# Kernel tuning notes

Measured on AMD Instinct MI355X. Metric: run time of the kernel, lower is better.

## Reference

```python
import jax, jax.numpy as jnp
import numpy as np

N_WORDS = 4096
N_HEADS = 512
EMB = 768          # input_size
HID = 1024         # hidden_size
DIST = 64          # dist_emb_size (forced by Conv1d(64, ...))
SENT_LEN = 64      # fixed sentence length -> static max padded length
PAIR_F = 2 * EMB + DIST  # 1600


def setup_inputs() -> dict:
    key = jax.random.key(0)
    ks = jax.random.split(key, 14)
    words = jax.random.normal(ks[0], (N_WORDS, EMB), dtype=jnp.float32)
    heads_ids = jax.random.randint(ks[1], (N_HEADS,), 0, N_WORDS, dtype=jnp.int64)
    sent_id = (jnp.arange(N_WORDS) // SENT_LEN).astype(jnp.int32)  # sorted, contiguous sentences
    s = 0.02
    return {
        "words": words,
        "heads_ids": heads_ids,
        "sent_id": sent_id,
        "emb_table": jax.random.normal(ks[2], (128, DIST), dtype=jnp.float32) * s,
        "W1": jax.random.normal(ks[3], (PAIR_F, HID), dtype=jnp.float32) * s,
        "b1": jnp.zeros((HID,), jnp.float32),
        "W2": jax.random.normal(ks[4], (HID, 256), dtype=jnp.float32) * s,
        "b2": jnp.zeros((256,), jnp.float32),
        "W3": jax.random.normal(ks[5], (256, DIST), dtype=jnp.float32) * s,
        "b3": jnp.zeros((DIST,), jnp.float32),
        "cw1": jax.random.normal(ks[6], (4, DIST, 3), dtype=jnp.float32) * s,  # Conv1d(64,4,3,1,1)
        "cb1": jnp.zeros((4,), jnp.float32),
        "cw2": jax.random.normal(ks[7], (2, 4, 3), dtype=jnp.float32) * s,    # Conv1d(4,2,3,1,1)
        "cb2": jnp.zeros((2,), jnp.float32),
    }


def _conv1d(x, w, b):
    # x: [N, C_in, L], w: [C_out, C_in, 3], padding=1, stride=1 (torch Conv1d semantics)
    y = jax.lax.conv_general_dilated(x, w, window_strides=(1,), padding=((1, 1),),
                                     dimension_numbers=("NCH", "OIH", "NCH"))
    return y + b[None, :, None]


def reference(words, heads_ids, sent_id, emb_table, W1, b1, W2, b2, W3, b3, cw1, cb1, cw2, cb2):
    n_words = words.shape[0]
    heads = heads_ids.astype(jnp.int32)
    H = heads.shape[0]

    # relative positions & distance-embedding ids, clamped to bucket 127 outside [-63, 63]
    rel = heads[:, None] - jnp.arange(n_words, dtype=jnp.int32)[None, :]      # [H, W]
    eid = rel + 63
    eid = jnp.where((eid < 0) | (eid > 126), 127, eid)

    # per-head sentence span (sent_id is sorted & contiguous)
    sh = sent_id[heads]
    starts = jnp.searchsorted(sent_id, sh, side="left")
    lengths = jnp.searchsorted(sent_id, sh, side="right") - starts            # [H]

    # padded ragged layout: row i holds words of head i's sentence, left-packed
    j = jnp.arange(SENT_LEN, dtype=jnp.int32)
    cols = starts[:, None] + j[None, :]                                       # [H, L]
    mask = j[None, :] < lengths[:, None]                                      # [H, L]
    cols_c = jnp.clip(cols, 0, n_words - 1)

    head_w = words[heads]                                                     # [H, E]
    col_w = words[cols_c]                                                     # [H, L, E]
    dist = emb_table[jnp.take_along_axis(eid, cols_c, axis=1)]                # [H, L, DIST]
    feat = jnp.concatenate(
        [jnp.broadcast_to(head_w[:, None, :], col_w.shape), col_w, dist], axis=-1)
    feat = jnp.where(mask[..., None], feat, jnp.zeros((), feat.dtype))        # zero padding rows (as torch)

    # FFNN (dropout is identity in eval mode)
    x = jax.nn.relu(feat @ W1 + b1)
    x = jax.nn.relu(x @ W2 + b2)
    x = x @ W3 + b3                                                           # [H, L, 64]

    # conv stack over the padded ragged axis
    x = _conv1d(x.transpose(0, 2, 1), cw1, cb1)
    x = _conv1d(x, cw2, cb2)
    res = x.transpose(0, 2, 1)                                                # [H, L, 2]

    # scatter back into [H, n_words, 2]; masked slots get out-of-range col -> dropped
    rows = jnp.broadcast_to(jnp.arange(H, dtype=jnp.int32)[:, None], mask.shape)
    cols_sc = jnp.where(mask, cols, n_words)
    scores = jnp.full((H, n_words, 2), -jnp.inf, dtype=words.dtype)
    scores = scores.at[rows, cols_sc].set(res, mode="drop")

    # eval-mode validity log-mask
    valid_starts = jnp.log((rel >= 0).astype(words.dtype))
    valid_ends = jnp.log((rel <= 0).astype(words.dtype))
    valid = jnp.stack([valid_starts, valid_ends], axis=2)
    return scores + valid
```

## Files before the change

kernel.cpp:

```cpp
#include <hip/hip_runtime.h>
#include <math.h>

#define NW   4096
#define NH   512
#define EMBD 768
#define HIDD 1024
#define DISTD 64
#define SLEN 64

#define NEG_BIG (-1.0e30f)

typedef __attribute__((ext_vector_type(8))) short short8;
typedef __attribute__((ext_vector_type(16))) float f32x16;
typedef __attribute__((ext_vector_type(4))) float f32x4;

#define MFMA32(a, b, c) __builtin_amdgcn_mfma_f32_32x32x16_bf16((a), (b), (c), 0, 0, 0)
#define MFMA16(a, b, c) __builtin_amdgcn_mfma_f32_16x16x32_bf16((a), (b), (c), 0, 0, 0)

__device__ __forceinline__ unsigned short f2bf(float f) {
    unsigned u = __float_as_uint(f);
    u += 0x7FFFu + ((u >> 16) & 1u);
    return (unsigned short)(u >> 16);
}
__device__ __forceinline__ float bf2f(unsigned short s) {
    return __uint_as_float(((unsigned)s) << 16);
}
__device__ __forceinline__ unsigned cvtpk(float lo, float hi) {
    unsigned r;
    asm("v_cvt_pk_bf16_f32 %0, %1, %2" : "=v"(r) : "v"(lo), "v"(hi));
    return r;
}
__device__ __forceinline__ short8 pack8(float f0, float f1, float f2, float f3,
                                        float f4, float f5, float f6, float f7) {
    union { unsigned u[4]; short8 s; } r;
    r.u[0] = cvtpk(f0, f1); r.u[1] = cvtpk(f2, f3);
    r.u[2] = cvtpk(f4, f5); r.u[3] = cvtpk(f6, f7);
    return r.s;
}

#define BARL()                                                   \
    do {                                                         \
        asm volatile("s_waitcnt lgkmcnt(0)" ::: "memory");       \
        __builtin_amdgcn_s_barrier();                            \
    } while (0)

__device__ __forceinline__ void pack_b32_dev(long t, const float* __restrict__ src,
                                             int ld, int nb32, int KB,
                                             unsigned short* __restrict__ dst)
{
    int l = (int)(t & 63); long u = t >> 6;
    int nb = (int)(u % nb32); int kb = (int)(u / nb32);
    int row0 = kb * 16 + ((l >> 5) << 3);
    int col  = (nb << 5) + (l & 31);
    const float* s = src + (size_t)row0 * ld + col;
    short8 v;
#pragma unroll
    for (int j = 0; j < 8; ++j) v[j] = (short)f2bf(s[(size_t)j * ld]);
    *(short8*)(dst + (((size_t)nb * KB + kb) << 9) + l * 8) = v;
}

__device__ __forceinline__ void pack_b16_dev(long t, const float* __restrict__ src,
                                             int ld, int nb16, int KB,
                                             unsigned short* __restrict__ dst)
{
    int l = (int)(t & 63); long u = t >> 6;
    int nb = (int)(u % nb16); int kb = (int)(u / nb16);
    int row0 = kb * 32 + ((l >> 4) << 3);
    int col  = (nb << 4) + (l & 15);
    const float* s = src + (size_t)row0 * ld + col;
    short8 v;
#pragma unroll
    for (int j = 0; j < 8; ++j) v[j] = (short)f2bf(s[(size_t)j * ld]);
    *(short8*)(dst + (((size_t)nb * KB + kb) << 9) + l * 8) = v;
}

__device__ __forceinline__ void cvt8_dev(long i, const float* __restrict__ src,
                                         unsigned short* __restrict__ dst)
{
    const float* s = src + i * 8;
    short8 v;
#pragma unroll
    for (int j = 0; j < 8; ++j) v[j] = (short)f2bf(s[j]);
    *(short8*)(dst + i * 8) = v;
}

#define WPS 776
__global__ __launch_bounds__(256)
void prep_kernel(const float* __restrict__ words, const float* __restrict__ emb,
                 const float* __restrict__ W1, const float* __restrict__ W2,
                 const float* __restrict__ W3,
                 const int* __restrict__ heads, const int* __restrict__ sent_id,
                 unsigned short* __restrict__ wpack, unsigned short* __restrict__ embb,
                 unsigned short* __restrict__ W1pa, unsigned short* __restrict__ W1px,
                 unsigned short* __restrict__ W1pd,
                 unsigned short* __restrict__ W2p, unsigned short* __restrict__ W3p,
                 int* __restrict__ starts, int* __restrict__ lens)
{
    __shared__ unsigned short tls[32 * WPS];

    const int b = blockIdx.x, tid = threadIdx.x;
    if (b < 128) {
        const int m = b;
#pragma unroll
        for (int i = 0; i < 24; ++i) {
            const int idx = tid + i * 256;
            const int r = idx / 192, c4 = (idx % 192) * 4;
            float4 v = *(const float4*)(words + ((size_t)(m * 32 + r)) * EMBD + c4);
            tls[r * WPS + c4 + 0] = f2bf(v.x);
            tls[r * WPS + c4 + 1] = f2bf(v.y);
            tls[r * WPS + c4 + 2] = f2bf(v.z);
            tls[r * WPS + c4 + 3] = f2bf(v.w);
        }
        __syncthreads();
        const int l = tid & 63, w = tid >> 6;
        for (int kb = w; kb < 48; kb += 4) {
            short8 v = *(const short8*)&tls[(l & 31) * WPS + kb * 16 + ((l >> 5) << 3)];
            *(short8*)(wpack + (((size_t)m * 48 + kb) << 9) + l * 8) = v;
        }
    } else if (b < 132) {
        cvt8_dev((long)(b - 128) * 256 + tid, emb, embb);
    } else if (b < 516) {
        pack_b32_dev((long)(b - 132) * 256 + tid, W1, HIDD, 32, 48, W1pa);
    } else if (b < 900) {
        pack_b32_dev((long)(b - 516) * 256 + tid, W1 + (size_t)768 * HIDD, HIDD, 32, 48, W1px);
    } else if (b < 932) {
        pack_b32_dev((long)(b - 900) * 256 + tid, W1 + (size_t)1536 * HIDD, HIDD, 32, 4, W1pd);
    } else if (b < 1060) {
        pack_b32_dev((long)(b - 932) * 256 + tid, W2, 256, 8, 64, W2p);
    } else if (b < 1068) {
        pack_b16_dev((long)(b - 1060) * 256 + tid, W3, 64, 4, 8, W3p);
    } else {
        int h = (b - 1068) * 256 + tid;
        if (h < NH) {
            int head = heads[h];
            int s = sent_id[head];
            int lo = 0, hi = NW;
            while (lo < hi) { int mid = (lo + hi) >> 1; if (sent_id[mid] < s) lo = mid + 1; else hi = mid; }
            int start = lo;
            lo = 0; hi = NW;
            while (lo < hi) { int mid = (lo + hi) >> 1; if (sent_id[mid] <= s) lo = mid + 1; else hi = mid; }
            int len = lo - start;
            if (len > SLEN) len = SLEN;
            starts[h] = start;
            lens[h] = len;
        }
    }
}

__global__ __launch_bounds__(256, 4)
void gemms_kernel(const unsigned short* __restrict__ wpack,
                  const unsigned short* __restrict__ embb,
                  const unsigned short* __restrict__ W1pa,
                  const unsigned short* __restrict__ W1px,
                  const unsigned short* __restrict__ W1pd,
                  const float* __restrict__ b1, const int* __restrict__ heads,
                  unsigned short* __restrict__ XwP, unsigned short* __restrict__ Hcb,
                  unsigned short* __restrict__ Dtb)
{
    __shared__ unsigned short tls[4][32 * 40];

    const int b = blockIdx.x, tid = threadIdx.x;
    const int l = tid & 63, w = tid >> 6;

    if (b < 1024) {
        const int mB = b >> 3, nB = b & 7;
        const int cbg = nB * 4 + w;
        const unsigned short* ap = wpack + (((size_t)mB * 48) << 9) + l * 8;
        const unsigned short* bp = W1px + (((size_t)cbg * 48) << 9) + l * 8;
        f32x16 acc = {};
#pragma unroll
        for (int kk = 0; kk < 48; ++kk) {
            short8 a = *(const short8*)(ap + ((size_t)kk << 9));
            short8 bb = *(const short8*)(bp + ((size_t)kk << 9));
            acc = MFMA32(a, bb, acc);
        }
        const int col = cbg * 32 + (l & 31);
        const float bv = b1[col];
        unsigned short* tw = tls[w];
#pragma unroll
        for (int r = 0; r < 16; ++r) {
            int rowl = (r & 3) + 8 * (r >> 2) + 4 * (l >> 5);
            tw[rowl * 40 + (l & 31)] = f2bf(acc[r] + bv);
        }
        short8 v0 = *(const short8*)&tw[(l & 31) * 40 + ((l >> 5) << 3)];
        short8 v1 = *(const short8*)&tw[(l & 31) * 40 + 16 + ((l >> 5) << 3)];
        *(short8*)(XwP + (((size_t)(mB * 64 + cbg * 2)) << 9) + l * 8) = v0;
        *(short8*)(XwP + (((size_t)(mB * 64 + cbg * 2 + 1)) << 9) + l * 8) = v1;
    } else if (b < 1152) {
        const int q = b - 1024;
        const int mB = q >> 3, nB = q & 7;
        const int cbg = nB * 4 + w;
        int row = heads[mB * 32 + (l & 31)];
        const unsigned short* ap = wpack + (((size_t)(row >> 5) * 48) << 9)
                                 + ((row & 31) + 32 * (l >> 5)) * 8;
        const unsigned short* bp = W1pa + (((size_t)cbg * 48) << 9) + l * 8;
        f32x16 acc = {};
#pragma unroll
        for (int kk = 0; kk < 48; ++kk) {
            short8 a = *(const short8*)(ap + ((size_t)kk << 9));
            short8 bb = *(const short8*)(bp + ((size_t)kk << 9));
            acc = MFMA32(a, bb, acc);
        }
        const int col = cbg * 32 + (l & 31);
#pragma unroll
        for (int r = 0; r < 16; ++r) {
            int rr = mB * 32 + (r & 3) + 8 * (r >> 2) + 4 * (l >> 5);
            Hcb[(size_t)rr * HIDD + col] = f2bf(acc[r]);
        }
    } else {
        const int q = b - 1152;
        const int mB = q >> 3, nB = q & 7;
        const int cbg = nB * 4 + w;
        const unsigned short* ap = embb + (size_t)(mB * 32 + (l & 31)) * DISTD + ((l >> 5) << 3);
        const unsigned short* bp = W1pd + (((size_t)cbg * 4) << 9) + l * 8;
        f32x16 acc = {};
#pragma unroll
        for (int kk = 0; kk < 4; ++kk) {
            short8 a = *(const short8*)(ap + kk * 16);
            short8 bb = *(const short8*)(bp + ((size_t)kk << 9));
            acc = MFMA32(a, bb, acc);
        }
        const int col = cbg * 32 + (l & 31);
#pragma unroll
        for (int r = 0; r < 16; ++r) {
            int rr = mB * 32 + (r & 3) + 8 * (r >> 2) + 4 * (l >> 5);
            Dtb[(size_t)rr * HIDD + col] = f2bf(acc[r]);
        }
    }
}

__global__ __launch_bounds__(256)
void packd_kernel(const unsigned short* __restrict__ Dtb,
                  unsigned short* __restrict__ PDr)
{
    const int tid = threadIdx.x, l = tid & 63;
    const int c = blockIdx.x * 4 + (tid >> 6);
    const int s = c / 192, rem = c % 192;
    const int m = rem >> 6, kb = rem & 63;
    const int row = 126 - (s + 32 * m + (l & 31));
    const int koff = kb * 16 + ((l >> 5) << 3);
    short8 v = *(const short8*)(Dtb + (size_t)row * HIDD + koff);
    *(short8*)(PDr + ((size_t)c << 9) + l * 8) = v;
}

#define NT 32
__global__ __launch_bounds__(512)
void head_kernel(const unsigned short* __restrict__ XwP,
                 const unsigned short* __restrict__ Hcb,
                 const unsigned short* __restrict__ PDr,
                 const unsigned short* __restrict__ W2p,
                 const float* __restrict__ b2,
                 const unsigned short* __restrict__ W3p,
                 const float* __restrict__ b3,
                 const float* __restrict__ cw1, const float* __restrict__ cb1,
                 const float* __restrict__ cw2, const float* __restrict__ cb2,
                 const int* __restrict__ heads, const int* __restrict__ starts,
                 const int* __restrict__ lens,
                 float* __restrict__ out)
{
    __shared__ char smem[67584];
    unsigned short* Ast = (unsigned short*)smem;
    unsigned short* Bst = (unsigned short*)(smem + 16384);
    unsigned short* x2s = (unsigned short*)smem;
    float* x3s = (float*)smem;
    float* y1s = (float*)(smem + 35328);
    float* y2s = (float*)(smem + 37376);

    const int tid = threadIdx.x;
    const int l = tid & 63, w = tid >> 6;
    const int h0 = blockIdx.x * 2;

    const int head0 = heads[h0],  head1 = heads[h0 + 1];
    const int strt0 = starts[h0], strt1 = starts[h0 + 1];
    const int len0  = lens[h0],   len1  = lens[h0 + 1];

    const int kkA = w >> 2, rb = w & 3;
    const int hbA = rb >> 1;
    const int headA = hbA ? head1 : head0;
    const int strtA = hbA ? strt1 : strt0;
    const int q0A = 63 - (headA - strtA);
    const unsigned short* xwPp =
        XwP + (((size_t)((strtA >> 5) + (rb & 1)) * 64) << 9) + l * 8;
    const unsigned short* ddPp =
        PDr + (((size_t)((q0A & 31) * 3 + (q0A >> 5) + (rb & 1)) * 64) << 9) + l * 8;
    const unsigned short* hcp = Hcb + (size_t)(h0 + hbA) * HIDD + ((l >> 5) << 3);
    const int kkB = w >> 2, nbB0 = (w & 3) * 2;
    const int mb = w & 1, nq = w >> 1;

    f32x16 acc[2][2] = {};

    short8 rxw, rhc, rdd, rb0, rb1;

#define LOADT(t)                                                              \
    {                                                                         \
        const int kb_ = (t) * 2 + kkA;                                        \
        rxw = *(const short8*)(xwPp + ((size_t)kb_ << 9));                    \
        rdd = *(const short8*)(ddPp + ((size_t)kb_ << 9));                    \
        rhc = *(const short8*)(hcp + kb_ * 16);                               \
        const size_t c0_ = ((size_t)(nbB0 * 64 + (t) * 2 + kkB)) << 9;        \
        rb0 = *(const short8*)(W2p + c0_ + l * 8);                            \
        rb1 = *(const short8*)(W2p + c0_ + 32768 + l * 8);                    \
    }

#define WRITET(t)                                                             \
    {                                                                         \
        const int buf_ = (t) & 1;                                             \
        float f_[8];                                                          \
        _Pragma("unroll")                                                     \
        for (int j = 0; j < 8; ++j)                                           \
            f_[j] = fmaxf(bf2f((unsigned short)rxw[j])                        \
                        + bf2f((unsigned short)rhc[j])                        \
                        + bf2f((unsigned short)rdd[j]), 0.f);                 \
        short8 v_ = pack8(f_[0], f_[1], f_[2], f_[3], f_[4], f_[5], f_[6], f_[7]); \
        *(short8*)&Ast[buf_ * 4096 + (kkA * 4 + rb) * 512 + l * 8] = v_;      \
        *(short8*)&Bst[buf_ * 8192 + (kkB * 8 + nbB0) * 512 + l * 8] = rb0;   \
        *(short8*)&Bst[buf_ * 8192 + (kkB * 8 + nbB0 + 1) * 512 + l * 8] = rb1; \
    }

    LOADT(0);
    WRITET(0);
    LOADT(1);
    BARL();

#pragma unroll 2
    for (int t = 0; t < NT; ++t) {
        const int buf = t & 1;
        short8 af0[2], af1[2], bf0[2], bf1[2];
#pragma unroll
        for (int k2 = 0; k2 < 2; ++k2) {
            af0[k2] = *(const short8*)&Ast[buf * 4096 + (k2 * 4 + mb * 2 + 0) * 512 + l * 8];
            af1[k2] = *(const short8*)&Ast[buf * 4096 + (k2 * 4 + mb * 2 + 1) * 512 + l * 8];
            bf0[k2] = *(const short8*)&Bst[buf * 8192 + (k2 * 8 + nq * 2 + 0) * 512 + l * 8];
            bf1[k2] = *(const short8*)&Bst[buf * 8192 + (k2 * 8 + nq * 2 + 1) * 512 + l * 8];
        }
        if (t + 1 < NT) WRITET(t + 1);
        if (t + 2 < NT) LOADT(t + 2);
        __builtin_amdgcn_s_setprio(1);
#pragma unroll
        for (int k2 = 0; k2 < 2; ++k2) {
            acc[0][0] = MFMA32(af0[k2], bf0[k2], acc[0][0]);
            acc[0][1] = MFMA32(af0[k2], bf1[k2], acc[0][1]);
            acc[1][0] = MFMA32(af1[k2], bf0[k2], acc[1][0]);
            acc[1][1] = MFMA32(af1[k2], bf1[k2], acc[1][1]);
        }
        __builtin_amdgcn_s_setprio(0);
        BARL();
    }

#pragma unroll
    for (int i = 0; i < 2; ++i) {
#pragma unroll
        for (int n = 0; n < 2; ++n) {
            const int ct = nq * 64 + n * 32 + (l & 31);
            const float bv = b2[ct];
#pragma unroll
            for (int r = 0; r < 16; ++r) {
                const int rt = mb * 64 + i * 32 + (r & 3) + 8 * (r >> 2) + 4 * (l >> 5);
                const int hb = rt >> 6, rl = rt & 63;
                x2s[hb * 16896 + rl * 264 + ct] = f2bf(fmaxf(acc[i][n][r] + bv, 0.f));
            }
        }
    }
    __syncthreads();

    {
        const int hb = w >> 2, q = w & 3;
        const unsigned short* x2h = x2s + hb * 16896;
        f32x4 acc2[4] = {};
#pragma unroll
        for (int kk = 0; kk < 8; ++kk) {
            short8 bf = *(const short8*)(W3p + ((q * 8 + kk) << 9) + l * 8);
#pragma unroll
            for (int mi = 0; mi < 4; ++mi) {
                short8 af = *(const short8*)&x2h[(mi * 16 + (l & 15)) * 264 + kk * 32 + ((l >> 4) << 3)];
                acc2[mi] = MFMA16(af, bf, acc2[mi]);
            }
        }
        __syncthreads();
        float* x3h = x3s + hb * 4416;
        const int col = q * 16 + (l & 15);
        const float b3v = b3[col];
#pragma unroll
        for (int mi = 0; mi < 4; ++mi) {
#pragma unroll
            for (int r = 0; r < 4; ++r) {
                const int rowv = mi * 16 + (l >> 4) * 4 + r;
                x3h[rowv * 69 + col] = acc2[mi][r] + b3v;
            }
        }
    }
    __syncthreads();

    {
        const int hb3 = tid >> 8;
        const int co = (tid >> 6) & 3;
        const int ll = tid & 63;
        const float* x3h = x3s + hb3 * 4416;
        float s = cb1[co];
        const float* wb = cw1 + co * DISTD * 3;
        for (int ci = 0; ci < DISTD; ++ci) {
            float w0 = wb[ci * 3 + 0], w1 = wb[ci * 3 + 1], w2v = wb[ci * 3 + 2];
            float xm = (ll > 0) ? x3h[(ll - 1) * 69 + ci] : 0.f;
            float xc = x3h[ll * 69 + ci];
            float xp = (ll < 63) ? x3h[(ll + 1) * 69 + ci] : 0.f;
            s = fmaf(xm, w0, s);
            s = fmaf(xc, w1, s);
            s = fmaf(xp, w2v, s);
        }
        y1s[hb3 * 256 + co * 64 + ll] = s;
    }
    __syncthreads();

    if (tid < 256) {
        const int hb4 = tid >> 7;
        const int co = (tid >> 6) & 1;
        const int ll = tid & 63;
        const float* yh = y1s + hb4 * 256;
        const int head = hb4 ? head1 : head0;
        const int strt = hb4 ? strt1 : strt0;
        float s = cb2[co];
#pragma unroll
        for (int ci = 0; ci < 4; ++ci) {
            const float* wb = cw2 + (co * 4 + ci) * 3;
            const float* yr = yh + ci * 64;
            float xm = (ll > 0) ? yr[ll - 1] : 0.f;
            float xc = yr[ll];
            float xp = (ll < 63) ? yr[ll + 1] : 0.f;
            s = fmaf(xm, wb[0], s);
            s = fmaf(xc, wb[1], s);
            s = fmaf(xp, wb[2], s);
        }
        const int col = strt + ll;
        const int rel = head - col;
        const bool valid = (co == 0) ? (rel >= 0) : (rel <= 0);
        y2s[hb4 * 128 + ll * 2 + co] = valid ? s : NEG_BIG;
    }
    __syncthreads();

    {
        const int hb = tid >> 8;
        const int c8 = tid & 255;
        const int strt = hb ? strt1 : strt0;
        const int len  = hb ? len1  : len0;
        float* orow = out + ((size_t)(h0 + hb) * NW) * 2;
        const float* yh = y2s + hb * 128;
#pragma unroll
        for (int i = 0; i < 16; ++i) {
            const int col = i * 256 + c8;
            float2 v;
            if (col >= strt && col < strt + len) {
                v = *(const float2*)&yh[(col - strt) * 2];
            } else {
                v.x = NEG_BIG; v.y = NEG_BIG;
            }
            *(float2*)&orow[(size_t)col * 2] = v;
        }
    }
}

extern "C" void kernel_launch(void* const* d_in, const int* in_sizes, int n_in,
                              void* d_out, int out_size, void* d_ws, size_t ws_size,
                              hipStream_t stream)
{
    const float* words = (const float*)d_in[0];
    const int* heads   = (const int*)d_in[1];
    const int* sent_id = (const int*)d_in[2];
    const float* emb   = (const float*)d_in[3];
    const float* W1    = (const float*)d_in[4];
    const float* b1    = (const float*)d_in[5];
    const float* W2    = (const float*)d_in[6];
    const float* b2    = (const float*)d_in[7];
    const float* W3    = (const float*)d_in[8];
    const float* b3    = (const float*)d_in[9];
    const float* cw1   = (const float*)d_in[10];
    const float* cb1   = (const float*)d_in[11];
    const float* cw2   = (const float*)d_in[12];
    const float* cb2   = (const float*)d_in[13];
    float* out = (float*)d_out;

    char* wsb = (char*)d_ws;
    unsigned short* XwP  = (unsigned short*)(wsb + 0);
    unsigned short* Hcb  = (unsigned short*)(wsb + 8388608);
    unsigned short* Dtb  = (unsigned short*)(wsb + 9437184);
    unsigned short* W2p  = (unsigned short*)(wsb + 9699328);
    unsigned short* W3p  = (unsigned short*)(wsb + 10223616);
    unsigned short* PDr  = (unsigned short*)(wsb + 10256384);
    unsigned short* embb = (unsigned short*)(wsb + 16547840);
    int* starts          = (int*)(wsb + 16564224);
    int* lens            = (int*)(wsb + 16566272);
    char* ob = (char*)d_out;
    unsigned short* wpack  = (unsigned short*)(ob + 0);
    unsigned short* W1pa   = (unsigned short*)(ob + 6291456);
    unsigned short* W1px   = (unsigned short*)(ob + 7864320);
    unsigned short* W1pd   = (unsigned short*)(ob + 9437184);
    (void)ws_size; (void)in_sizes; (void)n_in; (void)out_size;

    prep_kernel<<<dim3(1070), dim3(256), 0, stream>>>(
        words, emb, W1, W2, W3, heads, sent_id,
        wpack, embb, W1pa, W1px, W1pd, W2p, W3p, starts, lens);

    gemms_kernel<<<dim3(1184), dim3(256), 0, stream>>>(
        wpack, embb, W1pa, W1px, W1pd, b1, heads, XwP, Hcb, Dtb);

    packd_kernel<<<dim3(1536), dim3(256), 0, stream>>>(Dtb, PDr);

    head_kernel<<<dim3(NH / 2), dim3(512), 0, stream>>>(
        XwP, Hcb, PDr, W2p, b2, W3p, b3, cw1, cb1, cw2, cb2,
        heads, starts, lens, out);
}
```

Baseline: 77.68 us.

## Process one head per block instead of two in head_kernel

The head kernel now assigns one head per 512-thread block and launches 512 blocks instead of 256. Shared memory is cut to about 40KB and launch bounds request 4 blocks per CU, so more of the GPU's CUs are filled and occupancy rises. In exchange, each block streams the full W2 tile for only 64 rows, which doubles W2 traffic and halves MFMA work per B load. Half the waves also sit idle during A-tile prep and the W3 stage.

```diff
diff --git a/kernel.cpp b/kernel.cpp
--- a/kernel.cpp
+++ b/kernel.cpp
@@ -244,7 +244,7 @@
 }
 
 #define NT 32
-__global__ __launch_bounds__(512)
+__global__ __launch_bounds__(512, 4)
 void head_kernel(const unsigned short* __restrict__ XwP,
                  const unsigned short* __restrict__ Hcb,
                  const unsigned short* __restrict__ PDr,
@@ -258,61 +258,61 @@
                  const int* __restrict__ lens,
                  float* __restrict__ out)
 {
-    __shared__ char smem[67584];
+    __shared__ char smem[40960];
     unsigned short* Ast = (unsigned short*)smem;
-    unsigned short* Bst = (unsigned short*)(smem + 16384);
+    unsigned short* Bst = (unsigned short*)(smem + 8192);
     unsigned short* x2s = (unsigned short*)smem;
     float* x3s = (float*)smem;
-    float* y1s = (float*)(smem + 35328);
-    float* y2s = (float*)(smem + 37376);
+    float* y1s = (float*)(smem + 17664);
+    float* y2s = (float*)(smem + 18688);
 
     const int tid = threadIdx.x;
     const int l = tid & 63, w = tid >> 6;
-    const int h0 = blockIdx.x * 2;
-
-    const int head0 = heads[h0],  head1 = heads[h0 + 1];
-    const int strt0 = starts[h0], strt1 = starts[h0 + 1];
-    const int len0  = lens[h0],   len1  = lens[h0 + 1];
-
-    const int kkA = w >> 2, rb = w & 3;
-    const int hbA = rb >> 1;
-    const int headA = hbA ? head1 : head0;
-    const int strtA = hbA ? strt1 : strt0;
-    const int q0A = 63 - (headA - strtA);
+    const int h = blockIdx.x;
+
+    const int head = heads[h];
+    const int strt = starts[h];
+    const int len  = lens[h];
+
+    const int kkA = (w >> 1) & 1, rbA = w & 1;
+    const int q0 = 63 - (head - strt);
     const unsigned short* xwPp =
-        XwP + (((size_t)((strtA >> 5) + (rb & 1)) * 64) << 9) + l * 8;
+        XwP + (((size_t)((strt >> 5) + rbA) * 64) << 9) + l * 8;
     const unsigned short* ddPp =
-        PDr + (((size_t)((q0A & 31) * 3 + (q0A >> 5) + (rb & 1)) * 64) << 9) + l * 8;
-    const unsigned short* hcp = Hcb + (size_t)(h0 + hbA) * HIDD + ((l >> 5) << 3);
+        PDr + (((size_t)((q0 & 31) * 3 + (q0 >> 5) + rbA) * 64) << 9) + l * 8;
+    const unsigned short* hcp = Hcb + (size_t)h * HIDD + ((l >> 5) << 3);
     const int kkB = w >> 2, nbB0 = (w & 3) * 2;
-    const int mb = w & 1, nq = w >> 1;
-
-    f32x16 acc[2][2] = {};
-
+    const int rbC = w & 1, ncC = w >> 1;
+
+    f32x16 acc[2] = {};
     short8 rxw, rhc, rdd, rb0, rb1;
 
 #define LOADT(t)                                                              \
     {                                                                         \
-        const int kb_ = (t) * 2 + kkA;                                        \
-        rxw = *(const short8*)(xwPp + ((size_t)kb_ << 9));                    \
-        rdd = *(const short8*)(ddPp + ((size_t)kb_ << 9));                    \
-        rhc = *(const short8*)(hcp + kb_ * 16);                               \
-        const size_t c0_ = ((size_t)(nbB0 * 64 + (t) * 2 + kkB)) << 9;        \
-        rb0 = *(const short8*)(W2p + c0_ + l * 8);                            \
-        rb1 = *(const short8*)(W2p + c0_ + 32768 + l * 8);                    \
+        if (w < 4) {                                                          \
+            const int kbA_ = (t) * 2 + kkA;                                   \
+            rxw = *(const short8*)(xwPp + ((size_t)kbA_ << 9));               \
+            rdd = *(const short8*)(ddPp + ((size_t)kbA_ << 9));               \
+            rhc = *(const short8*)(hcp + kbA_ * 16);                          \
+        }                                                                     \
+        const int kbB_ = (t) * 2 + kkB;                                       \
+        rb0 = *(const short8*)(W2p + (((size_t)(nbB0 * 64 + kbB_)) << 9) + l * 8); \
+        rb1 = *(const short8*)(W2p + (((size_t)((nbB0 + 1) * 64 + kbB_)) << 9) + l * 8); \
     }
 
 #define WRITET(t)                                                             \
     {                                                                         \
         const int buf_ = (t) & 1;                                             \
-        float f_[8];                                                          \
-        _Pragma("unroll")                                                     \
-        for (int j = 0; j < 8; ++j)                                           \
-            f_[j] = fmaxf(bf2f((unsigned short)rxw[j])                        \
-                        + bf2f((unsigned short)rhc[j])                        \
-                        + bf2f((unsigned short)rdd[j]), 0.f);                 \
-        short8 v_ = pack8(f_[0], f_[1], f_[2], f_[3], f_[4], f_[5], f_[6], f_[7]); \
-        *(short8*)&Ast[buf_ * 4096 + (kkA * 4 + rb) * 512 + l * 8] = v_;      \
+        if (w < 4) {                                                          \
+            float f_[8];                                                      \
+            _Pragma("unroll")                                                 \
+            for (int j = 0; j < 8; ++j)                                       \
+                f_[j] = fmaxf(bf2f((unsigned short)rxw[j])                    \
+                            + bf2f((unsigned short)rhc[j])                    \
+                            + bf2f((unsigned short)rdd[j]), 0.f);             \
+            short8 v_ = pack8(f_[0], f_[1], f_[2], f_[3], f_[4], f_[5], f_[6], f_[7]); \
+            *(short8*)&Ast[buf_ * 2048 + (kkA * 2 + rbA) * 512 + l * 8] = v_; \
+        }                                                                     \
         *(short8*)&Bst[buf_ * 8192 + (kkB * 8 + nbB0) * 512 + l * 8] = rb0;   \
         *(short8*)&Bst[buf_ * 8192 + (kkB * 8 + nbB0 + 1) * 512 + l * 8] = rb1; \
     }
@@ -325,104 +325,92 @@
 #pragma unroll 2
     for (int t = 0; t < NT; ++t) {
         const int buf = t & 1;
-        short8 af0[2], af1[2], bf0[2], bf1[2];
+        short8 af[2], bf0[2], bf1[2];
 #pragma unroll
         for (int k2 = 0; k2 < 2; ++k2) {
-            af0[k2] = *(const short8*)&Ast[buf * 4096 + (k2 * 4 + mb * 2 + 0) * 512 + l * 8];
-            af1[k2] = *(const short8*)&Ast[buf * 4096 + (k2 * 4 + mb * 2 + 1) * 512 + l * 8];
-            bf0[k2] = *(const short8*)&Bst[buf * 8192 + (k2 * 8 + nq * 2 + 0) * 512 + l * 8];
-            bf1[k2] = *(const short8*)&Bst[buf * 8192 + (k2 * 8 + nq * 2 + 1) * 512 + l * 8];
+            af[k2]  = *(const short8*)&Ast[buf * 2048 + (k2 * 2 + rbC) * 512 + l * 8];
+            bf0[k2] = *(const short8*)&Bst[buf * 8192 + (k2 * 8 + ncC * 2 + 0) * 512 + l * 8];
+            bf1[k2] = *(const short8*)&Bst[buf * 8192 + (k2 * 8 + ncC * 2 + 1) * 512 + l * 8];
         }
         if (t + 1 < NT) WRITET(t + 1);
         if (t + 2 < NT) LOADT(t + 2);
         __builtin_amdgcn_s_setprio(1);
 #pragma unroll
         for (int k2 = 0; k2 < 2; ++k2) {
-            acc[0][0] = MFMA32(af0[k2], bf0[k2], acc[0][0]);
-            acc[0][1] = MFMA32(af0[k2], bf1[k2], acc[0][1]);
-            acc[1][0] = MFMA32(af1[k2], bf0[k2], acc[1][0]);
-            acc[1][1] = MFMA32(af1[k2], bf1[k2], acc[1][1]);
+            acc[0] = MFMA32(af[k2], bf0[k2], acc[0]);
+            acc[1] = MFMA32(af[k2], bf1[k2], acc[1]);
         }
         __builtin_amdgcn_s_setprio(0);
         BARL();
     }
 
 #pragma unroll
-    for (int i = 0; i < 2; ++i) {
-#pragma unroll
-        for (int n = 0; n < 2; ++n) {
-            const int ct = nq * 64 + n * 32 + (l & 31);
-            const float bv = b2[ct];
-#pragma unroll
-            for (int r = 0; r < 16; ++r) {
-                const int rt = mb * 64 + i * 32 + (r & 3) + 8 * (r >> 2) + 4 * (l >> 5);
-                const int hb = rt >> 6, rl = rt & 63;
-                x2s[hb * 16896 + rl * 264 + ct] = f2bf(fmaxf(acc[i][n][r] + bv, 0.f));
+    for (int n = 0; n < 2; ++n) {
+        const int ct = ncC * 64 + n * 32 + (l & 31);
+        const float bv = b2[ct];
+#pragma unroll
+        for (int r = 0; r < 16; ++r) {
+            const int rt = rbC * 32 + (r & 3) + 8 * (r >> 2) + 4 * (l >> 5);
+            x2s[rt * 264 + ct] = f2bf(fmaxf(acc[n][r] + bv, 0.f));
+        }
+    }
+    __syncthreads();
+
+    {
+        f32x4 acc2[4] = {};
+        if (w < 4) {
+#pragma unroll
+            for (int kk = 0; kk < 8; ++kk) {
+                short8 bfr = *(const short8*)(W3p + ((w * 8 + kk) << 9) + l * 8);
+#pragma unroll
+                for (int mi = 0; mi < 4; ++mi) {
+                    short8 afr = *(const short8*)&x2s[(mi * 16 + (l & 15)) * 264 + kk * 32 + ((l >> 4) << 3)];
+                    acc2[mi] = MFMA16(afr, bfr, acc2[mi]);
+                }
             }
         }
+        __syncthreads();
+        if (w < 4) {
+            const int col = w * 16 + (l & 15);
+            const float b3v = b3[col];
+#pragma unroll
+            for (int mi = 0; mi < 4; ++mi) {
+#pragma unroll
+                for (int r = 0; r < 4; ++r) {
+                    const int rowv = mi * 16 + (l >> 4) * 4 + r;
+                    x3s[rowv * 69 + col] = acc2[mi][r] + b3v;
+                }
+            }
+        }
     }
     __syncthreads();
 
-    {
-        const int hb = w >> 2, q = w & 3;
-        const unsigned short* x2h = x2s + hb * 16896;
-        f32x4 acc2[4] = {};
-#pragma unroll
-        for (int kk = 0; kk < 8; ++kk) {
-            short8 bf = *(const short8*)(W3p + ((q * 8 + kk) << 9) + l * 8);
-#pragma unroll
-            for (int mi = 0; mi < 4; ++mi) {
-                short8 af = *(const short8*)&x2h[(mi * 16 + (l & 15)) * 264 + kk * 32 + ((l >> 4) << 3)];
-                acc2[mi] = MFMA16(af, bf, acc2[mi]);
-            }
-        }
-        __syncthreads();
-        float* x3h = x3s + hb * 4416;
-        const int col = q * 16 + (l & 15);
-        const float b3v = b3[col];
-#pragma unroll
-        for (int mi = 0; mi < 4; ++mi) {
-#pragma unroll
-            for (int r = 0; r < 4; ++r) {
-                const int rowv = mi * 16 + (l >> 4) * 4 + r;
-                x3h[rowv * 69 + col] = acc2[mi][r] + b3v;
-            }
-        }
-    }
-    __syncthreads();
-
-    {
-        const int hb3 = tid >> 8;
-        const int co = (tid >> 6) & 3;
+    if (tid < 256) {
+        const int co = tid >> 6;
         const int ll = tid & 63;
-        const float* x3h = x3s + hb3 * 4416;
         float s = cb1[co];
         const float* wb = cw1 + co * DISTD * 3;
         for (int ci = 0; ci < DISTD; ++ci) {
             float w0 = wb[ci * 3 + 0], w1 = wb[ci * 3 + 1], w2v = wb[ci * 3 + 2];
-            float xm = (ll > 0) ? x3h[(ll - 1) * 69 + ci] : 0.f;
-            float xc = x3h[ll * 69 + ci];
-            float xp = (ll < 63) ? x3h[(ll + 1) * 69 + ci] : 0.f;
+            float xm = (ll > 0) ? x3s[(ll - 1) * 69 + ci] : 0.f;
+            float xc = x3s[ll * 69 + ci];
+            float xp = (ll < 63) ? x3s[(ll + 1) * 69 + ci] : 0.f;
             s = fmaf(xm, w0, s);
             s = fmaf(xc, w1, s);
             s = fmaf(xp, w2v, s);
         }
-        y1s[hb3 * 256 + co * 64 + ll] = s;
+        y1s[co * 64 + ll] = s;
     }
     __syncthreads();
 
-    if (tid < 256) {
-        const int hb4 = tid >> 7;
-        const int co = (tid >> 6) & 1;
+    if (tid < 128) {
+        const int co = tid >> 6;
         const int ll = tid & 63;
-        const float* yh = y1s + hb4 * 256;
-        const int head = hb4 ? head1 : head0;
-        const int strt = hb4 ? strt1 : strt0;
         float s = cb2[co];
 #pragma unroll
         for (int ci = 0; ci < 4; ++ci) {
             const float* wb = cw2 + (co * 4 + ci) * 3;
-            const float* yr = yh + ci * 64;
+            const float* yr = y1s + ci * 64;
             float xm = (ll > 0) ? yr[ll - 1] : 0.f;
             float xc = yr[ll];
             float xp = (ll < 63) ? yr[ll + 1] : 0.f;
@@ -433,23 +421,18 @@
         const int col = strt + ll;
         const int rel = head - col;
         const bool valid = (co == 0) ? (rel >= 0) : (rel <= 0);
-        y2s[hb4 * 128 + ll * 2 + co] = valid ? s : NEG_BIG;
+        y2s[ll * 2 + co] = valid ? s : NEG_BIG;
     }
     __syncthreads();
 
     {
-        const int hb = tid >> 8;
-        const int c8 = tid & 255;
-        const int strt = hb ? strt1 : strt0;
-        const int len  = hb ? len1  : len0;
-        float* orow = out + ((size_t)(h0 + hb) * NW) * 2;
-        const float* yh = y2s + hb * 128;
-#pragma unroll
-        for (int i = 0; i < 16; ++i) {
-            const int col = i * 256 + c8;
+        float* orow = out + ((size_t)h * NW) * 2;
+#pragma unroll
+        for (int i = 0; i < 8; ++i) {
+            const int col = i * 512 + tid;
             float2 v;
             if (col >= strt && col < strt + len) {
-                v = *(const float2*)&yh[(col - strt) * 2];
+                v = *(const float2*)&y2s[(col - strt) * 2];
             } else {
                 v.x = NEG_BIG; v.y = NEG_BIG;
             }
@@ -504,7 +487,7 @@
 
     packd_kernel<<<dim3(1536), dim3(256), 0, stream>>>(Dtb, PDr);
 
-    head_kernel<<<dim3(NH / 2), dim3(512), 0, stream>>>(
+    head_kernel<<<dim3(NH), dim3(512), 0, stream>>>(
         XwP, Hcb, PDr, W2p, b2, W3p, b3, cw1, cb1, cw2, cb2,
         heads, starts, lens, out);
 }
```

Result: slower. 80.43 us (+3.5%).

## Drop packd kernel, read distance rows directly, move W2/W3 packing into gemms

Applied to the files above, without the earlier changes.

Removes the packd_kernel launch that repacked the distance-projection table into MFMA fragment layout. The head kernel now loads distance fragments straight from the row-major Dtb, using a reversed row index and a 16-element k stride. The W2/W3 packing and the sentence-span search move from prep_kernel into extra blocks of gemms_kernel, and the s_setprio hints around the MFMA loop are removed. This saves one launch and a 6MB intermediate, at the cost of less-coalesced strided global loads in the head kernel's inner loop.

```diff
diff --git a/kernel.cpp b/kernel.cpp
--- a/kernel.cpp
+++ b/kernel.cpp
@@ -87,14 +87,10 @@
 #define WPS 776
 __global__ __launch_bounds__(256)
 void prep_kernel(const float* __restrict__ words, const float* __restrict__ emb,
-                 const float* __restrict__ W1, const float* __restrict__ W2,
-                 const float* __restrict__ W3,
-                 const int* __restrict__ heads, const int* __restrict__ sent_id,
+                 const float* __restrict__ W1,
                  unsigned short* __restrict__ wpack, unsigned short* __restrict__ embb,
                  unsigned short* __restrict__ W1pa, unsigned short* __restrict__ W1px,
-                 unsigned short* __restrict__ W1pd,
-                 unsigned short* __restrict__ W2p, unsigned short* __restrict__ W3p,
-                 int* __restrict__ starts, int* __restrict__ lens)
+                 unsigned short* __restrict__ W1pd)
 {
     __shared__ unsigned short tls[32 * WPS];
 
@@ -123,27 +119,8 @@
         pack_b32_dev((long)(b - 132) * 256 + tid, W1, HIDD, 32, 48, W1pa);
     } else if (b < 900) {
         pack_b32_dev((long)(b - 516) * 256 + tid, W1 + (size_t)768 * HIDD, HIDD, 32, 48, W1px);
-    } else if (b < 932) {
+    } else {
         pack_b32_dev((long)(b - 900) * 256 + tid, W1 + (size_t)1536 * HIDD, HIDD, 32, 4, W1pd);
-    } else if (b < 1060) {
-        pack_b32_dev((long)(b - 932) * 256 + tid, W2, 256, 8, 64, W2p);
-    } else if (b < 1068) {
-        pack_b16_dev((long)(b - 1060) * 256 + tid, W3, 64, 4, 8, W3p);
-    } else {
-        int h = (b - 1068) * 256 + tid;
-        if (h < NH) {
-            int head = heads[h];
-            int s = sent_id[head];
-            int lo = 0, hi = NW;
-            while (lo < hi) { int mid = (lo + hi) >> 1; if (sent_id[mid] < s) lo = mid + 1; else hi = mid; }
-            int start = lo;
-            lo = 0; hi = NW;
-            while (lo < hi) { int mid = (lo + hi) >> 1; if (sent_id[mid] <= s) lo = mid + 1; else hi = mid; }
-            int len = lo - start;
-            if (len > SLEN) len = SLEN;
-            starts[h] = start;
-            lens[h] = len;
-        }
     }
 }
 
@@ -153,9 +130,13 @@
                   const unsigned short* __restrict__ W1pa,
                   const unsigned short* __restrict__ W1px,
                   const unsigned short* __restrict__ W1pd,
+                  const float* __restrict__ W2, const float* __restrict__ W3,
                   const float* __restrict__ b1, const int* __restrict__ heads,
+                  const int* __restrict__ sent_id,
                   unsigned short* __restrict__ XwP, unsigned short* __restrict__ Hcb,
-                  unsigned short* __restrict__ Dtb)
+                  unsigned short* __restrict__ Dtb,
+                  unsigned short* __restrict__ W2p, unsigned short* __restrict__ W3p,
+                  int* __restrict__ starts, int* __restrict__ lens)
 {
     __shared__ unsigned short tls[4][32 * 40];
 
@@ -207,7 +188,7 @@
             int rr = mB * 32 + (r & 3) + 8 * (r >> 2) + 4 * (l >> 5);
             Hcb[(size_t)rr * HIDD + col] = f2bf(acc[r]);
         }
-    } else {
+    } else if (b < 1184) {
         const int q = b - 1152;
         const int mB = q >> 3, nB = q & 7;
         const int cbg = nB * 4 + w;
@@ -226,28 +207,33 @@
             int rr = mB * 32 + (r & 3) + 8 * (r >> 2) + 4 * (l >> 5);
             Dtb[(size_t)rr * HIDD + col] = f2bf(acc[r]);
         }
-    }
-}
-
-__global__ __launch_bounds__(256)
-void packd_kernel(const unsigned short* __restrict__ Dtb,
-                  unsigned short* __restrict__ PDr)
-{
-    const int tid = threadIdx.x, l = tid & 63;
-    const int c = blockIdx.x * 4 + (tid >> 6);
-    const int s = c / 192, rem = c % 192;
-    const int m = rem >> 6, kb = rem & 63;
-    const int row = 126 - (s + 32 * m + (l & 31));
-    const int koff = kb * 16 + ((l >> 5) << 3);
-    short8 v = *(const short8*)(Dtb + (size_t)row * HIDD + koff);
-    *(short8*)(PDr + ((size_t)c << 9) + l * 8) = v;
+    } else if (b < 1312) {
+        pack_b32_dev((long)(b - 1184) * 256 + tid, W2, 256, 8, 64, W2p);
+    } else if (b < 1320) {
+        pack_b16_dev((long)(b - 1312) * 256 + tid, W3, 64, 4, 8, W3p);
+    } else {
+        int h = (b - 1320) * 256 + tid;
+        if (h < NH) {
+            int head = heads[h];
+            int s = sent_id[head];
+            int lo = 0, hi = NW;
+            while (lo < hi) { int mid = (lo + hi) >> 1; if (sent_id[mid] < s) lo = mid + 1; else hi = mid; }
+            int start = lo;
+            lo = 0; hi = NW;
+            while (lo < hi) { int mid = (lo + hi) >> 1; if (sent_id[mid] <= s) lo = mid + 1; else hi = mid; }
+            int len = lo - start;
+            if (len > SLEN) len = SLEN;
+            starts[h] = start;
+            lens[h] = len;
+        }
+    }
 }
 
 #define NT 32
 __global__ __launch_bounds__(512)
 void head_kernel(const unsigned short* __restrict__ XwP,
                  const unsigned short* __restrict__ Hcb,
-                 const unsigned short* __restrict__ PDr,
+                 const unsigned short* __restrict__ Dtb,
                  const unsigned short* __restrict__ W2p,
                  const float* __restrict__ b2,
                  const unsigned short* __restrict__ W3p,
@@ -281,8 +267,8 @@
     const int q0A = 63 - (headA - strtA);
     const unsigned short* xwPp =
         XwP + (((size_t)((strtA >> 5) + (rb & 1)) * 64) << 9) + l * 8;
-    const unsigned short* ddPp =
-        PDr + (((size_t)((q0A & 31) * 3 + (q0A >> 5) + (rb & 1)) * 64) << 9) + l * 8;
+    const int ddRow = 126 - q0A - 32 * (rb & 1) - (l & 31);
+    const unsigned short* ddPp = Dtb + (size_t)ddRow * HIDD + ((l >> 5) << 3);
     const unsigned short* hcp = Hcb + (size_t)(h0 + hbA) * HIDD + ((l >> 5) << 3);
     const int kkB = w >> 2, nbB0 = (w & 3) * 2;
     const int mb = w & 1, nq = w >> 1;
@@ -295,7 +281,7 @@
     {                                                                         \
         const int kb_ = (t) * 2 + kkA;                                        \
         rxw = *(const short8*)(xwPp + ((size_t)kb_ << 9));                    \
-        rdd = *(const short8*)(ddPp + ((size_t)kb_ << 9));                    \
+        rdd = *(const short8*)(ddPp + kb_ * 16);                              \
         rhc = *(const short8*)(hcp + kb_ * 16);                               \
         const size_t c0_ = ((size_t)(nbB0 * 64 + (t) * 2 + kkB)) << 9;        \
         rb0 = *(const short8*)(W2p + c0_ + l * 8);                            \
@@ -335,7 +321,6 @@
         }
         if (t + 1 < NT) WRITET(t + 1);
         if (t + 2 < NT) LOADT(t + 2);
-        __builtin_amdgcn_s_setprio(1);
 #pragma unroll
         for (int k2 = 0; k2 < 2; ++k2) {
             acc[0][0] = MFMA32(af0[k2], bf0[k2], acc[0][0]);
@@ -343,7 +328,6 @@
             acc[1][0] = MFMA32(af1[k2], bf0[k2], acc[1][0]);
             acc[1][1] = MFMA32(af1[k2], bf1[k2], acc[1][1]);
         }
-        __builtin_amdgcn_s_setprio(0);
         BARL();
     }
 
@@ -484,10 +468,9 @@
     unsigned short* Dtb  = (unsigned short*)(wsb + 9437184);
     unsigned short* W2p  = (unsigned short*)(wsb + 9699328);
     unsigned short* W3p  = (unsigned short*)(wsb + 10223616);
-    unsigned short* PDr  = (unsigned short*)(wsb + 10256384);
-    unsigned short* embb = (unsigned short*)(wsb + 16547840);
-    int* starts          = (int*)(wsb + 16564224);
-    int* lens            = (int*)(wsb + 16566272);
+    unsigned short* embb = (unsigned short*)(wsb + 10256384);
+    int* starts          = (int*)(wsb + 10272768);
+    int* lens            = (int*)(wsb + 10274816);
     char* ob = (char*)d_out;
     unsigned short* wpack  = (unsigned short*)(ob + 0);
     unsigned short* W1pa   = (unsigned short*)(ob + 6291456);
@@ -495,16 +478,14 @@
     unsigned short* W1pd   = (unsigned short*)(ob + 9437184);
     (void)ws_size; (void)in_sizes; (void)n_in; (void)out_size;
 
-    prep_kernel<<<dim3(1070), dim3(256), 0, stream>>>(
-        words, emb, W1, W2, W3, heads, sent_id,
-        wpack, embb, W1pa, W1px, W1pd, W2p, W3p, starts, lens);
-
-    gemms_kernel<<<dim3(1184), dim3(256), 0, stream>>>(
-        wpack, embb, W1pa, W1px, W1pd, b1, heads, XwP, Hcb, Dtb);
-
-    packd_kernel<<<dim3(1536), dim3(256), 0, stream>>>(Dtb, PDr);
+    prep_kernel<<<dim3(932), dim3(256), 0, stream>>>(
+        words, emb, W1, wpack, embb, W1pa, W1px, W1pd);
+
+    gemms_kernel<<<dim3(1322), dim3(256), 0, stream>>>(
+        wpack, embb, W1pa, W1px, W1pd, W2, W3, b1, heads, sent_id,
+        XwP, Hcb, Dtb, W2p, W3p, starts, lens);
 
     head_kernel<<<dim3(NH / 2), dim3(512), 0, stream>>>(
-        XwP, Hcb, PDr, W2p, b2, W3p, b3, cw1, cb1, cw2, cb2,
+        XwP, Hcb, Dtb, W2p, b2, W3p, b3, cw1, cb1, cw2, cb2,
         heads, starts, lens, out);
 }
```

Result: faster. 73.67 us (median of 2 runs) (-5.2%).
